# Kernel tuning notes

Measured on AMD Instinct MI355X. Metric: run time of the kernel, lower is better.

The kernel has to match this reference:

```python
import jax, jax.numpy as jnp
import numpy as np

CONF_THRESH = 0.01
TOP_K = 200
NMS_THRESH = 0.45


def setup_inputs() -> dict:
    key = jax.random.key(0)
    k1, k2, k3, k4, k5 = jax.random.split(key, 5)
    B, N, C = 32, 8732, 21
    return {
        "loc_data": jax.random.normal(k1, (B, N, 4), jnp.float32),
        "conf_data": jax.random.normal(k2, (B, N, C), jnp.float32),
        "loc_data2": jax.random.normal(k3, (B, N, 4), jnp.float32),
        "conf_data2": jax.random.normal(k4, (B, N, C), jnp.float32),
        "dbox_list": jax.random.uniform(k5, (N, 4), jnp.float32),
    }


def decode(loc, dbox):
    # SSD decode with variances (0.1, 0.2); loc,dbox: [N,4]; returns xyxy
    cxcy = dbox[:, :2] + loc[:, :2] * 0.1 * dbox[:, 2:]
    wh = dbox[:, 2:] * jnp.exp(loc[:, 2:] * 0.2)
    return jnp.concatenate([cxcy - wh * 0.5, cxcy + wh * 0.5], axis=-1)


def iou_matrix(b):
    # b: [K,4] xyxy -> [K,K] IoU
    x1 = jnp.maximum(b[:, None, 0], b[None, :, 0])
    y1 = jnp.maximum(b[:, None, 1], b[None, :, 1])
    x2 = jnp.minimum(b[:, None, 2], b[None, :, 2])
    y2 = jnp.minimum(b[:, None, 3], b[None, :, 3])
    inter = jnp.clip(x2 - x1, 0.0) * jnp.clip(y2 - y1, 0.0)
    area = (b[:, 2] - b[:, 0]) * (b[:, 3] - b[:, 1])
    union = area[:, None] + area[None, :] - inter
    return inter / union


def nms_class(scores, boxes):
    # scores: [M], boxes: [M,4] for one (image, class)
    masked = jnp.where(scores > CONF_THRESH, scores, -1.0)  # drop sub-threshold
    cand_s, idx = jax.lax.top_k(masked, TOP_K)              # top_k candidate pool
    cand_b = boxes[idx]
    valid = cand_s > CONF_THRESH
    iou = iou_matrix(cand_b)

    def step(suppressed, j):
        keep_j = valid[j] & (~suppressed[j])
        suppressed = suppressed | (keep_j & (iou[j] > NMS_THRESH))
        return suppressed, keep_j

    _, keep = jax.lax.scan(step, jnp.zeros((TOP_K,), bool), jnp.arange(TOP_K))
    entries = jnp.concatenate([cand_s[:, None], cand_b], axis=1)  # [K,5] = (score, box)
    pos = jnp.cumsum(keep) - 1
    pos = jnp.where(keep, pos, TOP_K)  # out-of-bounds -> dropped
    return jnp.zeros((TOP_K, 5), entries.dtype).at[pos].set(entries, mode="drop")


def reference(loc_data, conf_data, loc_data2, conf_data2, dbox_list):
    B, N, _ = loc_data.shape
    C = conf_data.shape[2]
    conf = jax.nn.softmax(conf_data, axis=-1)    # [B,N,C]
    conf2 = jax.nn.softmax(conf_data2, axis=-1)
    boxes1 = jax.vmap(decode, in_axes=(0, None))(loc_data, dbox_list)   # [B,N,4]
    boxes2 = jax.vmap(decode, in_axes=(0, None))(loc_data2, dbox_list)
    # horizontal flip of second (TTA) view: x1' = 1 - x2, x2' = 1 - x1
    boxes2 = jnp.stack(
        [1.0 - boxes2[..., 2], boxes2[..., 1], 1.0 - boxes2[..., 0], boxes2[..., 3]],
        axis=-1,
    )
    boxes = jnp.concatenate([boxes1, boxes2], axis=1)   # [B,2N,4]
    scores = jnp.concatenate([conf, conf2], axis=1)     # [B,2N,C]
    scores = jnp.moveaxis(scores, -1, 1)                # [B,C,2N]
    # vmap over batch and (non-background) classes
    per_class = jax.vmap(jax.vmap(nms_class, in_axes=(0, None)), in_axes=(0, 0))(
        scores[:, 1:], boxes
    )  # [B,C-1,TOP_K,5]
    out = jnp.zeros((B, C, TOP_K, 5), loc_data.dtype)
    return out.at[:, 1:].set(per_class)
```

## Files before the change

### kernel.cpp

```cpp
#include <hip/hip_runtime.h>

#define B_ 32
#define N_ 8732
#define N2_ 17464
#define N4_ 4366
#define C_ 21
#define NCLS 20
#define K_ 200
#define CONF_T 0.01f
#define NMS_T 0.45f
#define TPB_S 256
#define TPB_N 512
#define POOL 1024
#define RANKCAP 512
#define HB0 2048
#define HB 1024
#define BIN0 30791u

typedef unsigned long long u64;
typedef unsigned int u32;

__global__ __launch_bounds__(TPB_S) void softmax_kernel(
    const float* __restrict__ conf1, const float* __restrict__ conf2,
    float* __restrict__ scores)
{
  __shared__ float lds[TPB_S * C_];
  const int t = threadIdx.x;
  const int tile = blockIdx.x * TPB_S;
  const int b = blockIdx.y;
  const int view = blockIdx.z;
  int cnt = N_ - tile; if (cnt > TPB_S) cnt = TPB_S;
  const float* conf = view ? conf2 : conf1;
  const float4* src = (const float4*)(conf + ((size_t)b * N_ + tile) * C_);
  float4* l4 = (float4*)lds;
  const int n4 = (cnt * C_) >> 2;
  for (int i = t; i < n4; i += TPB_S) l4[i] = src[i];
  __syncthreads();
  if (t < cnt) {
    float x[C_];
#pragma unroll
    for (int i = 0; i < C_; ++i) x[i] = lds[t * C_ + i];
    float m = x[0];
#pragma unroll
    for (int i = 1; i < C_; ++i) m = fmaxf(m, x[i]);
    float e[C_];
    float sum = 0.0f;
#pragma unroll
    for (int i = 0; i < C_; ++i) { e[i] = __expf(x[i] - m); sum += e[i]; }
    float inv = 1.0f / sum;
    float* o = scores + ((size_t)b * NCLS) * N2_ + (size_t)view * N_ + (tile + t);
#pragma unroll
    for (int c = 1; c < C_; ++c) { *o = e[c] * inv; o += N2_; }
  }
}

__global__ __launch_bounds__(TPB_N, 2) void nms_kernel(
    const float* __restrict__ scores,
    const float4* __restrict__ loc1,
    const float4* __restrict__ loc2,
    const float4* __restrict__ dbox,
    float* __restrict__ out)
{
  const int t = threadIdx.x;
  const int lane = t & 63;
  const int wv = t >> 6;
  const int bimg = blockIdx.x / NCLS;
  const int cls = 1 + (blockIdx.x % NCLS);
  const float4* sc4 = (const float4*)(scores + ((size_t)bimg * NCLS + (cls - 1)) * N2_);
  float* ob = out + ((size_t)bimg * C_ + cls) * K_ * 5;

  __shared__ u32 hist[HB0];
  __shared__ u64 pool[POOL] __attribute__((aligned(16)));
  __shared__ u64 spool[256];
  __shared__ float4 bb[K_];
  __shared__ float bar[K_];
  __shared__ u64 rowmask[K_][4];
  __shared__ u64 validmask[4];
  __shared__ u32 wtot[8];
  __shared__ u32 sh_sel, sh_Sb, sh_Sn, sh_nc;

  {
    const float4 z4 = make_float4(0.f, 0.f, 0.f, 0.f);
    if (t < 250) ((float4*)ob)[t] = z4;
    if (cls == 1 && t >= 256 && t < 506)
      ((float4*)(out + (size_t)bimg * C_ * K_ * 5))[t - 256] = z4;
  }

  float4 v[9];
#pragma unroll
  for (int k = 0; k < 9; ++k) {
    int i = t + k * TPB_N;
    v[k] = (i < N4_) ? sc4[i] : make_float4(0.f, 0.f, 0.f, 0.f);
  }

  hist[t] = 0u; hist[t + 512] = 0u; hist[t + 1024] = 0u; hist[t + 1536] = 0u;
  pool[t] = 0ULL; pool[t + TPB_N] = 0ULL;
  if (t == 0) sh_nc = 0u;
  __syncthreads();

#pragma unroll
  for (int k = 0; k < 9; ++k) {
    float ss[4] = {v[k].x, v[k].y, v[k].z, v[k].w};
#pragma unroll
    for (int c2 = 0; c2 < 4; ++c2) {
      float s = ss[c2];
      if (s > CONF_T)
        atomicAdd(&hist[(__float_as_uint(s) >> 15) - BIN0], 1u);
    }
  }
  __syncthreads();

  {
    u32 c0 = hist[4 * t + 0], c1 = hist[4 * t + 1];
    u32 c2b = hist[4 * t + 2], c3 = hist[4 * t + 3];
    u32 T = c0 + c1 + c2b + c3;
    u32 x = T;
#pragma unroll
    for (int off = 1; off < 64; off <<= 1) {
      u32 y = __shfl_down(x, off);
      if (lane + off < 64) x += y;
    }
    if (lane == 0) wtot[wv] = x;
    __syncthreads();
    u32 wafter = 0;
    for (int w = wv + 1; w < 8; ++w) wafter += wtot[w];
    u32 after_me = (x - T) + wafter;
    u32 S3 = c3 + after_me, S2 = c2b + S3, S1 = c1 + S2, S0 = c0 + S1;
    hist[4 * t + 0] = S0; hist[4 * t + 1] = S1;
    hist[4 * t + 2] = S2; hist[4 * t + 3] = S3;
  }
  __syncthreads();

  u32 loKey, prefix = 0, Gacc = 0;
  bool needMore = false;
  {
    u32 total = hist[0];
    if (total < (u32)K_) {
      loKey = 1u;
    } else {
      for (int h = t; h < HB0; h += TPB_N) {
        u32 Sb = hist[h];
        u32 Sn = (h + 1 < HB0) ? hist[h + 1] : 0u;
        if (Sb >= (u32)K_ && Sn < (u32)K_) { sh_sel = (u32)h; sh_Sb = Sb; sh_Sn = Sn; }
      }
      __syncthreads();
      prefix = sh_sel + BIN0;
      loKey = prefix << 15;
      Gacc = sh_Sn;
      needMore = sh_Sb > (u32)RANKCAP;
    }
  }

  for (int lvl = 1; lvl <= 2 && needMore; ++lvl) {
    const int shift = (lvl == 1) ? 5 : 0;
    const int mshift = (lvl == 1) ? 15 : 5;
    const u32 bmask = (lvl == 1) ? 1023u : 31u;
    for (int h = t; h < HB; h += TPB_N) hist[h] = 0u;
    __syncthreads();
#pragma unroll
    for (int k = 0; k < 9; ++k) {
      float ss[4] = {v[k].x, v[k].y, v[k].z, v[k].w};
#pragma unroll
      for (int c2 = 0; c2 < 4; ++c2) {
        float s = ss[c2];
        if (s > CONF_T) {
          u32 key = __float_as_uint(s);
          if ((key >> mshift) == prefix)
            atomicAdd(&hist[(key >> shift) & bmask], 1u);
        }
      }
    }
    __syncthreads();
    u32 c0 = hist[2 * t], c1 = hist[2 * t + 1];
    u32 T = c0 + c1;
    u32 x = T;
#pragma unroll
    for (int off = 1; off < 64; off <<= 1) {
      u32 y = __shfl_down(x, off);
      if (lane + off < 64) x += y;
    }
    if (lane == 0) wtot[wv] = x;
    __syncthreads();
    u32 wafter = 0;
    for (int w = wv + 1; w < 8; ++w) wafter += wtot[w];
    u32 after_me = (x - T) + wafter;
    u32 S1 = c1 + after_me, S0 = c0 + S1;
    hist[2 * t] = S0; hist[2 * t + 1] = S1;
    __syncthreads();
    u32 need = (u32)K_ - Gacc;
    for (int h = t; h < HB; h += TPB_N) {
      u32 Sb = hist[h];
      u32 Sn2 = (h + 1 < HB) ? hist[h + 1] : 0u;
      if (Sb >= need && Sn2 < need) { sh_sel = (u32)h; sh_Sb = Sb; sh_Sn = Sn2; }
    }
    __syncthreads();
    prefix = (prefix << ((lvl == 1) ? 10 : 5)) | sh_sel;
    u32 candTotal = Gacc + sh_Sb;
    Gacc += sh_Sn;
    loKey = prefix << shift;
    needMore = (candTotal > (u32)RANKCAP) && (lvl < 2);
  }

#pragma unroll
  for (int k = 0; k < 9; ++k) {
    int i = t + k * TPB_N;
    float ss[4] = {v[k].x, v[k].y, v[k].z, v[k].w};
#pragma unroll
    for (int c2 = 0; c2 < 4; ++c2) {
      float s = ss[c2];
      u32 key = __float_as_uint(s);
      bool pred = (s > CONF_T) && (key >= loKey);
      u64 bal = __ballot(pred);
      if (bal) {
        u32 wb = 0;
        if (lane == 0) wb = atomicAdd(&sh_nc, (u32)__popcll(bal));
        wb = __shfl(wb, 0);
        if (pred) {
          u32 pos = wb + (u32)__popcll(bal & ((1ULL << lane) - 1ULL));
          if (pos < (u32)POOL)
            pool[pos] = ((u64)key << 32) | (u64)(0xFFFFFFFFu - (u32)(i * 4 + c2));
        }
      }
    }
  }
  __syncthreads();

  u32 nc = sh_nc < (u32)POOL ? sh_nc : (u32)POOL;
  if (t < 256) spool[t] = 0ULL;
  const bool dual = nc > (u32)TPB_N;
  u64 my0 = (t < (int)nc) ? pool[t] : 0ULL;
  u64 my1 = (dual && t + TPB_N < (int)nc) ? pool[t + TPB_N] : 0ULL;
  __syncthreads();
  u32 r0 = 0, r1 = 0;
  if ((u32)(t & ~63) < nc) {
    if (!dual) {
#pragma unroll 4
      for (u32 k = 0; k < nc; k += 2) {
        ulonglong2 pk = *(const ulonglong2*)&pool[k];
        r0 += (pk.x > my0) ? 1u : 0u;
        r0 += (pk.y > my0) ? 1u : 0u;
      }
    } else {
#pragma unroll 4
      for (u32 k = 0; k < nc; k += 2) {
        ulonglong2 pk = *(const ulonglong2*)&pool[k];
        r0 += (pk.x > my0) ? 1u : 0u;
        r0 += (pk.y > my0) ? 1u : 0u;
        r1 += (pk.x > my1) ? 1u : 0u;
        r1 += (pk.y > my1) ? 1u : 0u;
      }
    }
  }
  if (my0 != 0ULL && r0 < (u32)K_) spool[r0] = my0;
  if (dual && my1 != 0ULL && r1 < (u32)K_) spool[r1] = my1;
  __syncthreads();

  float scv = 0.f;
  if (t < K_) {
    float x1 = 0.f, y1 = 0.f, x2 = 0.f, y2 = 0.f, area = 0.f;
    u64 e = spool[t];
    u32 kb = (u32)(e >> 32);
    if (kb != 0u) {
      scv = __uint_as_float(kb);
      u32 idx = 0xFFFFFFFFu - (u32)(e & 0xFFFFFFFFu);
      int nn = (idx < (u32)N_) ? (int)idx : (int)(idx - N_);
      float4 l = (idx < (u32)N_) ? loc1[(size_t)bimg * N_ + nn]
                                 : loc2[(size_t)bimg * N_ + nn];
      float4 d = dbox[nn];
      float cx = d.x + l.x * 0.1f * d.z;
      float cy = d.y + l.y * 0.1f * d.w;
      float w = d.z * __expf(l.z * 0.2f);
      float h = d.w * __expf(l.w * 0.2f);
      x1 = cx - w * 0.5f; y1 = cy - h * 0.5f;
      x2 = cx + w * 0.5f; y2 = cy + h * 0.5f;
      if (idx >= (u32)N_) {
        float tmp = 1.0f - x2; x2 = 1.0f - x1; x1 = tmp;
      }
      area = (x2 - x1) * (y2 - y1);
    }
    bb[t] = make_float4(x1, y1, x2, y2);
    bar[t] = area;
  } else if (t >= 256) {
    for (int i = t - 256; i < 4 * K_; i += 256) ((u64*)rowmask)[i] = 0ULL;
  }
  {
    bool myvalid = (t < K_) && (scv > CONF_T);
    u64 bal = __ballot(myvalid);
    if (lane == 0 && wv < 4) validmask[wv] = bal;
  }
  __syncthreads();

  if (t < 2 * K_) {
    const int j = (t < K_) ? t : (t - K_);
    const int h = (t < K_) ? 0 : 1;
    const int L = K_ - 1 - j;
    const int half = (L + 1) >> 1;
    const int s0c = j + 1 + (h ? half : 0);
    const int e0c = h ? K_ : (j + 1 + half);
    if (s0c < e0c) {
      float4 mb = bb[j];
      float ma = bar[j];
      for (int w = (s0c >> 6); w <= ((e0c - 1) >> 6); ++w) {
        int ka = (w << 6) > s0c ? (w << 6) : s0c;
        int kb2 = ((w + 1) << 6) < e0c ? ((w + 1) << 6) : e0c;
        u64 m = 0ULL;
        for (int k2 = ka; k2 < kb2; ++k2) {
          float4 obx = bb[k2];
          float ox1 = fmaxf(mb.x, obx.x);
          float oy1 = fmaxf(mb.y, obx.y);
          float ox2 = fminf(mb.z, obx.z);
          float oy2 = fminf(mb.w, obx.w);
          float inter = fmaxf(ox2 - ox1, 0.f) * fmaxf(oy2 - oy1, 0.f);
          float uni = ma + bar[k2] - inter;
          m |= (inter > NMS_T * uni) ? (1ULL << (k2 & 63)) : 0ULL;
        }
        if (m) atomicOr(&rowmask[j][w], m);
      }
    }
  }
  __syncthreads();

  if (t < 64) {
    const u64 vv0 = validmask[0], vv1 = validmask[1];
    const u64 vv2 = validmask[2], vv3 = validmask[3];
    u64 s0 = 0, s1 = 0, s2 = 0, s3 = 0;
    u64 k0 = 0, k1 = 0, k2m = 0, k3 = 0;
#pragma unroll 8
    for (int j = 0; j < 64; ++j) {
      u64 q0 = rowmask[j][0], q1 = rowmask[j][1], q2 = rowmask[j][2], q3 = rowmask[j][3];
      u64 bit = 1ULL << j;
      if ((vv0 & bit) && !(s0 & bit)) { s0 |= q0; s1 |= q1; s2 |= q2; s3 |= q3; k0 |= bit; }
    }
#pragma unroll 8
    for (int j = 64; j < 128; ++j) {
      u64 q1 = rowmask[j][1], q2 = rowmask[j][2], q3 = rowmask[j][3];
      u64 bit = 1ULL << (j & 63);
      if ((vv1 & bit) && !(s1 & bit)) { s1 |= q1; s2 |= q2; s3 |= q3; k1 |= bit; }
    }
#pragma unroll 8
    for (int j = 128; j < 192; ++j) {
      u64 q2 = rowmask[j][2], q3 = rowmask[j][3];
      u64 bit = 1ULL << (j & 63);
      if ((vv2 & bit) && !(s2 & bit)) { s2 |= q2; s3 |= q3; k2m |= bit; }
    }
#pragma unroll
    for (int j = 192; j < K_; ++j) {
      u64 q3 = rowmask[j][3];
      u64 bit = 1ULL << (j & 63);
      if ((vv3 & bit) && !(s3 & bit)) { s3 |= q3; k3 |= bit; }
    }
    const u32 n0 = (u32)__popcll(k0);
    const u32 n01 = n0 + (u32)__popcll(k1);
    const u32 n012 = n01 + (u32)__popcll(k2m);
    const u64 below = (1ULL << lane) - 1ULL;
#pragma unroll
    for (int w = 0; w < 4; ++w) {
      int j = (w << 6) + lane;
      if (j < K_) {
        u64 kw = (w == 0) ? k0 : (w == 1) ? k1 : (w == 2) ? k2m : k3;
        if ((kw >> lane) & 1ULL) {
          int pos2 = (int)__popcll(kw & below)
                  + (int)((w == 0) ? 0u : (w == 1) ? n0 : (w == 2) ? n01 : n012);
          u64 e = spool[j];
          float sc = __uint_as_float((u32)(e >> 32));
          float4 bx = bb[j];
          float* o = ob + (size_t)pos2 * 5;
          o[0] = sc; o[1] = bx.x; o[2] = bx.y; o[3] = bx.z; o[4] = bx.w;
        }
      }
    }
  }
}

extern "C" void kernel_launch(void* const* d_in, const int* in_sizes, int n_in,
                              void* d_out, int out_size, void* d_ws, size_t ws_size,
                              hipStream_t stream) {
  const float* loc1 = (const float*)d_in[0];
  const float* conf1 = (const float*)d_in[1];
  const float* loc2 = (const float*)d_in[2];
  const float* conf2 = (const float*)d_in[3];
  const float* dbox = (const float*)d_in[4];
  float* out = (float*)d_out;
  float* scores = (float*)d_ws;

  dim3 g1((N_ + TPB_S - 1) / TPB_S, B_, 2);
  softmax_kernel<<<g1, TPB_S, 0, stream>>>(conf1, conf2, scores);

  nms_kernel<<<B_ * NCLS, TPB_N, 0, stream>>>(
      scores, (const float4*)loc1, (const float4*)loc2, (const float4*)dbox, out);
}
```

Measured before the change: 151.6 us.

## Replace radix refinement with histogram-bucketed scatter and per-bucket ranking

```diff
diff --git a/kernel.cpp b/kernel.cpp
--- a/kernel.cpp
+++ b/kernel.cpp
@@ -131,12 +131,13 @@
   }
   __syncthreads();
 
-  u32 loKey, prefix = 0, Gacc = 0;
-  bool needMore = false;
+  u32 loKey, selBin = 0, ncand, prefix = 0, Gacc = 0;
+  bool fallback = false;
   {
     u32 total = hist[0];
     if (total < (u32)K_) {
       loKey = 1u;
+      ncand = total;
     } else {
       for (int h = t; h < HB0; h += TPB_N) {
         u32 Sb = hist[h];
@@ -144,115 +145,144 @@
         if (Sb >= (u32)K_ && Sn < (u32)K_) { sh_sel = (u32)h; sh_Sb = Sb; sh_Sn = Sn; }
       }
       __syncthreads();
+      selBin = sh_sel;
       prefix = sh_sel + BIN0;
       loKey = prefix << 15;
+      ncand = sh_Sb;
       Gacc = sh_Sn;
-      needMore = sh_Sb > (u32)RANKCAP;
-    }
-  }
-
-  for (int lvl = 1; lvl <= 2 && needMore; ++lvl) {
-    const int shift = (lvl == 1) ? 5 : 0;
-    const int mshift = (lvl == 1) ? 15 : 5;
-    const u32 bmask = (lvl == 1) ? 1023u : 31u;
-    for (int h = t; h < HB; h += TPB_N) hist[h] = 0u;
-    __syncthreads();
+      fallback = sh_Sb > (u32)POOL;
+    }
+  }
+
+  if (t < 256) spool[t] = 0ULL;
+
+  if (!fallback) {
 #pragma unroll
     for (int k = 0; k < 9; ++k) {
+      int i = t + k * TPB_N;
       float ss[4] = {v[k].x, v[k].y, v[k].z, v[k].w};
 #pragma unroll
       for (int c2 = 0; c2 < 4; ++c2) {
         float s = ss[c2];
-        if (s > CONF_T) {
-          u32 key = __float_as_uint(s);
-          if ((key >> mshift) == prefix)
-            atomicAdd(&hist[(key >> shift) & bmask], 1u);
+        u32 key = __float_as_uint(s);
+        if (s > CONF_T && key >= loKey) {
+          u32 h = (key >> 15) - BIN0;
+          u32 pos = atomicSub(&hist[h], 1u) - 1u;
+          pool[pos] = ((u64)key << 32) | (u64)(0xFFFFFFFFu - (u32)(i * 4 + c2));
         }
       }
     }
     __syncthreads();
-    u32 c0 = hist[2 * t], c1 = hist[2 * t + 1];
-    u32 T = c0 + c1;
-    u32 x = T;
-#pragma unroll
-    for (int off = 1; off < 64; off <<= 1) {
-      u32 y = __shfl_down(x, off);
-      if (lane + off < 64) x += y;
-    }
-    if (lane == 0) wtot[wv] = x;
+    for (int slot = t; slot < (int)ncand; slot += TPB_N) {
+      u64 e = pool[slot];
+      u32 h = ((u32)(e >> 32) >> 15) - BIN0;
+      u32 base = hist[h];
+      u32 up = (h == selBin) ? ncand : hist[h - 1];
+      u32 r = base;
+      for (u32 q = base; q < up; ++q) r += (pool[q] > e) ? 1u : 0u;
+      if (r < (u32)K_) spool[r] = e;
+    }
+  } else {
+    bool needMore = true;
+    for (int lvl = 1; lvl <= 2 && needMore; ++lvl) {
+      const int shift = (lvl == 1) ? 5 : 0;
+      const int mshift = (lvl == 1) ? 15 : 5;
+      const u32 bmask = (lvl == 1) ? 1023u : 31u;
+      for (int h = t; h < HB; h += TPB_N) hist[h] = 0u;
+      __syncthreads();
+#pragma unroll
+      for (int k = 0; k < 9; ++k) {
+        float ss[4] = {v[k].x, v[k].y, v[k].z, v[k].w};
+#pragma unroll
+        for (int c2 = 0; c2 < 4; ++c2) {
+          float s = ss[c2];
+          if (s > CONF_T) {
+            u32 key = __float_as_uint(s);
+            if ((key >> mshift) == prefix)
+              atomicAdd(&hist[(key >> shift) & bmask], 1u);
+          }
+        }
+      }
+      __syncthreads();
+      u32 c0 = hist[2 * t], c1 = hist[2 * t + 1];
+      u32 T = c0 + c1;
+      u32 x = T;
+#pragma unroll
+      for (int off = 1; off < 64; off <<= 1) {
+        u32 y = __shfl_down(x, off);
+        if (lane + off < 64) x += y;
+      }
+      if (lane == 0) wtot[wv] = x;
+      __syncthreads();
+      u32 wafter = 0;
+      for (int w = wv + 1; w < 8; ++w) wafter += wtot[w];
+      u32 after_me = (x - T) + wafter;
+      u32 S1 = c1 + after_me, S0 = c0 + S1;
+      hist[2 * t] = S0; hist[2 * t + 1] = S1;
+      __syncthreads();
+      u32 need = (u32)K_ - Gacc;
+      for (int h = t; h < HB; h += TPB_N) {
+        u32 Sb = hist[h];
+        u32 Sn2 = (h + 1 < HB) ? hist[h + 1] : 0u;
+        if (Sb >= need && Sn2 < need) { sh_sel = (u32)h; sh_Sb = Sb; sh_Sn = Sn2; }
+      }
+      __syncthreads();
+      prefix = (prefix << ((lvl == 1) ? 10 : 5)) | sh_sel;
+      u32 candTotal = Gacc + sh_Sb;
+      Gacc += sh_Sn;
+      loKey = prefix << shift;
+      needMore = (candTotal > (u32)RANKCAP) && (lvl < 2);
+    }
+#pragma unroll
+    for (int k = 0; k < 9; ++k) {
+      int i = t + k * TPB_N;
+      float ss[4] = {v[k].x, v[k].y, v[k].z, v[k].w};
+#pragma unroll
+      for (int c2 = 0; c2 < 4; ++c2) {
+        float s = ss[c2];
+        u32 key = __float_as_uint(s);
+        bool pred = (s > CONF_T) && (key >= loKey);
+        u64 bal = __ballot(pred);
+        if (bal) {
+          u32 wb = 0;
+          if (lane == 0) wb = atomicAdd(&sh_nc, (u32)__popcll(bal));
+          wb = __shfl(wb, 0);
+          if (pred) {
+            u32 pos = wb + (u32)__popcll(bal & ((1ULL << lane) - 1ULL));
+            if (pos < (u32)POOL)
+              pool[pos] = ((u64)key << 32) | (u64)(0xFFFFFFFFu - (u32)(i * 4 + c2));
+          }
+        }
+      }
+    }
     __syncthreads();
-    u32 wafter = 0;
-    for (int w = wv + 1; w < 8; ++w) wafter += wtot[w];
-    u32 after_me = (x - T) + wafter;
-    u32 S1 = c1 + after_me, S0 = c0 + S1;
-    hist[2 * t] = S0; hist[2 * t + 1] = S1;
-    __syncthreads();
-    u32 need = (u32)K_ - Gacc;
-    for (int h = t; h < HB; h += TPB_N) {
-      u32 Sb = hist[h];
-      u32 Sn2 = (h + 1 < HB) ? hist[h + 1] : 0u;
-      if (Sb >= need && Sn2 < need) { sh_sel = (u32)h; sh_Sb = Sb; sh_Sn = Sn2; }
-    }
-    __syncthreads();
-    prefix = (prefix << ((lvl == 1) ? 10 : 5)) | sh_sel;
-    u32 candTotal = Gacc + sh_Sb;
-    Gacc += sh_Sn;
-    loKey = prefix << shift;
-    needMore = (candTotal > (u32)RANKCAP) && (lvl < 2);
-  }
-
-#pragma unroll
-  for (int k = 0; k < 9; ++k) {
-    int i = t + k * TPB_N;
-    float ss[4] = {v[k].x, v[k].y, v[k].z, v[k].w};
-#pragma unroll
-    for (int c2 = 0; c2 < 4; ++c2) {
-      float s = ss[c2];
-      u32 key = __float_as_uint(s);
-      bool pred = (s > CONF_T) && (key >= loKey);
-      u64 bal = __ballot(pred);
-      if (bal) {
-        u32 wb = 0;
-        if (lane == 0) wb = atomicAdd(&sh_nc, (u32)__popcll(bal));
-        wb = __shfl(wb, 0);
-        if (pred) {
-          u32 pos = wb + (u32)__popcll(bal & ((1ULL << lane) - 1ULL));
-          if (pos < (u32)POOL)
-            pool[pos] = ((u64)key << 32) | (u64)(0xFFFFFFFFu - (u32)(i * 4 + c2));
-        }
-      }
-    }
-  }
-  __syncthreads();
-
-  u32 nc = sh_nc < (u32)POOL ? sh_nc : (u32)POOL;
-  if (t < 256) spool[t] = 0ULL;
-  const bool dual = nc > (u32)TPB_N;
-  u64 my0 = (t < (int)nc) ? pool[t] : 0ULL;
-  u64 my1 = (dual && t + TPB_N < (int)nc) ? pool[t + TPB_N] : 0ULL;
-  __syncthreads();
-  u32 r0 = 0, r1 = 0;
-  if ((u32)(t & ~63) < nc) {
-    if (!dual) {
+    u32 nc = sh_nc < (u32)POOL ? sh_nc : (u32)POOL;
+    const bool dual = nc > (u32)TPB_N;
+    u64 my0 = (t < (int)nc) ? pool[t] : 0ULL;
+    u64 my1 = (dual && t + TPB_N < (int)nc) ? pool[t + TPB_N] : 0ULL;
+    u32 r0 = 0, r1 = 0;
+    if ((u32)(t & ~63) < nc) {
+      if (!dual) {
 #pragma unroll 4
-      for (u32 k = 0; k < nc; k += 2) {
-        ulonglong2 pk = *(const ulonglong2*)&pool[k];
-        r0 += (pk.x > my0) ? 1u : 0u;
-        r0 += (pk.y > my0) ? 1u : 0u;
-      }
-    } else {
+        for (u32 k = 0; k < nc; k += 2) {
+          ulonglong2 pk = *(const ulonglong2*)&pool[k];
+          r0 += (pk.x > my0) ? 1u : 0u;
+          r0 += (pk.y > my0) ? 1u : 0u;
+        }
+      } else {
 #pragma unroll 4
-      for (u32 k = 0; k < nc; k += 2) {
-        ulonglong2 pk = *(const ulonglong2*)&pool[k];
-        r0 += (pk.x > my0) ? 1u : 0u;
-        r0 += (pk.y > my0) ? 1u : 0u;
-        r1 += (pk.x > my1) ? 1u : 0u;
-        r1 += (pk.y > my1) ? 1u : 0u;
-      }
-    }
-  }
-  if (my0 != 0ULL && r0 < (u32)K_) spool[r0] = my0;
-  if (dual && my1 != 0ULL && r1 < (u32)K_) spool[r1] = my1;
+        for (u32 k = 0; k < nc; k += 2) {
+          ulonglong2 pk = *(const ulonglong2*)&pool[k];
+          r0 += (pk.x > my0) ? 1u : 0u;
+          r0 += (pk.y > my0) ? 1u : 0u;
+          r1 += (pk.x > my1) ? 1u : 0u;
+          r1 += (pk.y > my1) ? 1u : 0u;
+        }
+      }
+    }
+    if (my0 != 0ULL && r0 < (u32)K_) spool[r0] = my0;
+    if (dual && my1 != 0ULL && r1 < (u32)K_) spool[r1] = my1;
+  }
   __syncthreads();
 
   float scv = 0.f;
```

After: 145.3 us. -4.1%, faster.

## Make NMS kernel persistent with atomic work-stealing over image-class items

Applied to the files above, without the earlier changes.

```diff
diff --git a/kernel.cpp b/kernel.cpp
--- a/kernel.cpp
+++ b/kernel.cpp
@@ -7,6 +7,8 @@
 #define C_ 21
 #define NCLS 20
 #define K_ 200
+#define NITEMS 640
+#define PGRID 512
 #define CONF_T 0.01f
 #define NMS_T 0.45f
 #define TPB_S 256
@@ -22,13 +24,14 @@
 
 __global__ __launch_bounds__(TPB_S) void softmax_kernel(
     const float* __restrict__ conf1, const float* __restrict__ conf2,
-    float* __restrict__ scores)
+    float* __restrict__ scores, u32* gcnt)
 {
   __shared__ float lds[TPB_S * C_];
   const int t = threadIdx.x;
   const int tile = blockIdx.x * TPB_S;
   const int b = blockIdx.y;
   const int view = blockIdx.z;
+  if (gcnt && t == 0 && tile == 0 && b == 0 && view == 0) *gcnt = 0u;
   int cnt = N_ - tile; if (cnt > TPB_S) cnt = TPB_S;
   const float* conf = view ? conf2 : conf1;
   const float4* src = (const float4*)(conf + ((size_t)b * N_ + tile) * C_);
@@ -59,15 +62,11 @@
     const float4* __restrict__ loc1,
     const float4* __restrict__ loc2,
     const float4* __restrict__ dbox,
-    float* __restrict__ out)
+    float* __restrict__ out, u32* gcnt)
 {
   const int t = threadIdx.x;
   const int lane = t & 63;
   const int wv = t >> 6;
-  const int bimg = blockIdx.x / NCLS;
-  const int cls = 1 + (blockIdx.x % NCLS);
-  const float4* sc4 = (const float4*)(scores + ((size_t)bimg * NCLS + (cls - 1)) * N2_);
-  float* ob = out + ((size_t)bimg * C_ + cls) * K_ * 5;
 
   __shared__ u32 hist[HB0];
   __shared__ u64 pool[POOL] __attribute__((aligned(16)));
@@ -77,298 +76,313 @@
   __shared__ u64 rowmask[K_][4];
   __shared__ u64 validmask[4];
   __shared__ u32 wtot[8];
-  __shared__ u32 sh_sel, sh_Sb, sh_Sn, sh_nc;
-
-  {
-    const float4 z4 = make_float4(0.f, 0.f, 0.f, 0.f);
-    if (t < 250) ((float4*)ob)[t] = z4;
-    if (cls == 1 && t >= 256 && t < 506)
-      ((float4*)(out + (size_t)bimg * C_ * K_ * 5))[t - 256] = z4;
-  }
-
-  float4 v[9];
-#pragma unroll
-  for (int k = 0; k < 9; ++k) {
-    int i = t + k * TPB_N;
-    v[k] = (i < N4_) ? sc4[i] : make_float4(0.f, 0.f, 0.f, 0.f);
-  }
-
-  hist[t] = 0u; hist[t + 512] = 0u; hist[t + 1024] = 0u; hist[t + 1536] = 0u;
-  pool[t] = 0ULL; pool[t + TPB_N] = 0ULL;
-  if (t == 0) sh_nc = 0u;
-  __syncthreads();
-
-#pragma unroll
-  for (int k = 0; k < 9; ++k) {
-    float ss[4] = {v[k].x, v[k].y, v[k].z, v[k].w};
-#pragma unroll
-    for (int c2 = 0; c2 < 4; ++c2) {
-      float s = ss[c2];
-      if (s > CONF_T)
-        atomicAdd(&hist[(__float_as_uint(s) >> 15) - BIN0], 1u);
-    }
-  }
-  __syncthreads();
-
-  {
-    u32 c0 = hist[4 * t + 0], c1 = hist[4 * t + 1];
-    u32 c2b = hist[4 * t + 2], c3 = hist[4 * t + 3];
-    u32 T = c0 + c1 + c2b + c3;
-    u32 x = T;
-#pragma unroll
-    for (int off = 1; off < 64; off <<= 1) {
-      u32 y = __shfl_down(x, off);
-      if (lane + off < 64) x += y;
-    }
-    if (lane == 0) wtot[wv] = x;
-    __syncthreads();
-    u32 wafter = 0;
-    for (int w = wv + 1; w < 8; ++w) wafter += wtot[w];
-    u32 after_me = (x - T) + wafter;
-    u32 S3 = c3 + after_me, S2 = c2b + S3, S1 = c1 + S2, S0 = c0 + S1;
-    hist[4 * t + 0] = S0; hist[4 * t + 1] = S1;
-    hist[4 * t + 2] = S2; hist[4 * t + 3] = S3;
-  }
-  __syncthreads();
-
-  u32 loKey, prefix = 0, Gacc = 0;
-  bool needMore = false;
-  {
-    u32 total = hist[0];
-    if (total < (u32)K_) {
-      loKey = 1u;
-    } else {
-      for (int h = t; h < HB0; h += TPB_N) {
-        u32 Sb = hist[h];
-        u32 Sn = (h + 1 < HB0) ? hist[h + 1] : 0u;
-        if (Sb >= (u32)K_ && Sn < (u32)K_) { sh_sel = (u32)h; sh_Sb = Sb; sh_Sn = Sn; }
-      }
-      __syncthreads();
-      prefix = sh_sel + BIN0;
-      loKey = prefix << 15;
-      Gacc = sh_Sn;
-      needMore = sh_Sb > (u32)RANKCAP;
-    }
-  }
-
-  for (int lvl = 1; lvl <= 2 && needMore; ++lvl) {
-    const int shift = (lvl == 1) ? 5 : 0;
-    const int mshift = (lvl == 1) ? 15 : 5;
-    const u32 bmask = (lvl == 1) ? 1023u : 31u;
-    for (int h = t; h < HB; h += TPB_N) hist[h] = 0u;
-    __syncthreads();
+  __shared__ u32 sh_sel, sh_Sb, sh_Sn, sh_nc, sh_item;
+
+  u32 item = blockIdx.x;
+
+  while (true) {
+    const int bimg = (int)(item / NCLS);
+    const int cls = 1 + (int)(item % NCLS);
+    const float4* sc4 = (const float4*)(scores + ((size_t)bimg * NCLS + (cls - 1)) * N2_);
+    float* ob = out + ((size_t)bimg * C_ + cls) * K_ * 5;
+
+    {
+      const float4 z4 = make_float4(0.f, 0.f, 0.f, 0.f);
+      if (t < 250) ((float4*)ob)[t] = z4;
+      if (cls == 1 && t >= 256 && t < 506)
+        ((float4*)(out + (size_t)bimg * C_ * K_ * 5))[t - 256] = z4;
+    }
+
+    float4 v[9];
+#pragma unroll
+    for (int k = 0; k < 9; ++k) {
+      int i = t + k * TPB_N;
+      v[k] = (i < N4_) ? sc4[i] : make_float4(0.f, 0.f, 0.f, 0.f);
+    }
+
+    hist[t] = 0u; hist[t + 512] = 0u; hist[t + 1024] = 0u; hist[t + 1536] = 0u;
+    pool[t] = 0ULL; pool[t + TPB_N] = 0ULL;
+    if (t == 0) sh_nc = 0u;
+    __syncthreads();
+
 #pragma unroll
     for (int k = 0; k < 9; ++k) {
       float ss[4] = {v[k].x, v[k].y, v[k].z, v[k].w};
 #pragma unroll
       for (int c2 = 0; c2 < 4; ++c2) {
         float s = ss[c2];
-        if (s > CONF_T) {
-          u32 key = __float_as_uint(s);
-          if ((key >> mshift) == prefix)
-            atomicAdd(&hist[(key >> shift) & bmask], 1u);
-        }
-      }
-    }
-    __syncthreads();
-    u32 c0 = hist[2 * t], c1 = hist[2 * t + 1];
-    u32 T = c0 + c1;
-    u32 x = T;
-#pragma unroll
-    for (int off = 1; off < 64; off <<= 1) {
-      u32 y = __shfl_down(x, off);
-      if (lane + off < 64) x += y;
-    }
-    if (lane == 0) wtot[wv] = x;
-    __syncthreads();
-    u32 wafter = 0;
-    for (int w = wv + 1; w < 8; ++w) wafter += wtot[w];
-    u32 after_me = (x - T) + wafter;
-    u32 S1 = c1 + after_me, S0 = c0 + S1;
-    hist[2 * t] = S0; hist[2 * t + 1] = S1;
-    __syncthreads();
-    u32 need = (u32)K_ - Gacc;
-    for (int h = t; h < HB; h += TPB_N) {
-      u32 Sb = hist[h];
-      u32 Sn2 = (h + 1 < HB) ? hist[h + 1] : 0u;
-      if (Sb >= need && Sn2 < need) { sh_sel = (u32)h; sh_Sb = Sb; sh_Sn = Sn2; }
-    }
-    __syncthreads();
-    prefix = (prefix << ((lvl == 1) ? 10 : 5)) | sh_sel;
-    u32 candTotal = Gacc + sh_Sb;
-    Gacc += sh_Sn;
-    loKey = prefix << shift;
-    needMore = (candTotal > (u32)RANKCAP) && (lvl < 2);
-  }
-
-#pragma unroll
-  for (int k = 0; k < 9; ++k) {
-    int i = t + k * TPB_N;
-    float ss[4] = {v[k].x, v[k].y, v[k].z, v[k].w};
-#pragma unroll
-    for (int c2 = 0; c2 < 4; ++c2) {
-      float s = ss[c2];
-      u32 key = __float_as_uint(s);
-      bool pred = (s > CONF_T) && (key >= loKey);
-      u64 bal = __ballot(pred);
-      if (bal) {
-        u32 wb = 0;
-        if (lane == 0) wb = atomicAdd(&sh_nc, (u32)__popcll(bal));
-        wb = __shfl(wb, 0);
-        if (pred) {
-          u32 pos = wb + (u32)__popcll(bal & ((1ULL << lane) - 1ULL));
-          if (pos < (u32)POOL)
-            pool[pos] = ((u64)key << 32) | (u64)(0xFFFFFFFFu - (u32)(i * 4 + c2));
-        }
-      }
-    }
-  }
-  __syncthreads();
-
-  u32 nc = sh_nc < (u32)POOL ? sh_nc : (u32)POOL;
-  if (t < 256) spool[t] = 0ULL;
-  const bool dual = nc > (u32)TPB_N;
-  u64 my0 = (t < (int)nc) ? pool[t] : 0ULL;
-  u64 my1 = (dual && t + TPB_N < (int)nc) ? pool[t + TPB_N] : 0ULL;
-  __syncthreads();
-  u32 r0 = 0, r1 = 0;
-  if ((u32)(t & ~63) < nc) {
-    if (!dual) {
+        if (s > CONF_T)
+          atomicAdd(&hist[(__float_as_uint(s) >> 15) - BIN0], 1u);
+      }
+    }
+    __syncthreads();
+
+    {
+      u32 c0 = hist[4 * t + 0], c1 = hist[4 * t + 1];
+      u32 c2b = hist[4 * t + 2], c3 = hist[4 * t + 3];
+      u32 T = c0 + c1 + c2b + c3;
+      u32 x = T;
+#pragma unroll
+      for (int off = 1; off < 64; off <<= 1) {
+        u32 y = __shfl_down(x, off);
+        if (lane + off < 64) x += y;
+      }
+      if (lane == 0) wtot[wv] = x;
+      __syncthreads();
+      u32 wafter = 0;
+      for (int w = wv + 1; w < 8; ++w) wafter += wtot[w];
+      u32 after_me = (x - T) + wafter;
+      u32 S3 = c3 + after_me, S2 = c2b + S3, S1 = c1 + S2, S0 = c0 + S1;
+      hist[4 * t + 0] = S0; hist[4 * t + 1] = S1;
+      hist[4 * t + 2] = S2; hist[4 * t + 3] = S3;
+    }
+    __syncthreads();
+
+    u32 loKey, prefix = 0, Gacc = 0;
+    bool needMore = false;
+    {
+      u32 total = hist[0];
+      if (total < (u32)K_) {
+        loKey = 1u;
+      } else {
+        for (int h = t; h < HB0; h += TPB_N) {
+          u32 Sb = hist[h];
+          u32 Sn = (h + 1 < HB0) ? hist[h + 1] : 0u;
+          if (Sb >= (u32)K_ && Sn < (u32)K_) { sh_sel = (u32)h; sh_Sb = Sb; sh_Sn = Sn; }
+        }
+        __syncthreads();
+        prefix = sh_sel + BIN0;
+        loKey = prefix << 15;
+        Gacc = sh_Sn;
+        needMore = sh_Sb > (u32)RANKCAP;
+      }
+    }
+
+    for (int lvl = 1; lvl <= 2 && needMore; ++lvl) {
+      const int shift = (lvl == 1) ? 5 : 0;
+      const int mshift = (lvl == 1) ? 15 : 5;
+      const u32 bmask = (lvl == 1) ? 1023u : 31u;
+      for (int h = t; h < HB; h += TPB_N) hist[h] = 0u;
+      __syncthreads();
+#pragma unroll
+      for (int k = 0; k < 9; ++k) {
+        float ss[4] = {v[k].x, v[k].y, v[k].z, v[k].w};
+#pragma unroll
+        for (int c2 = 0; c2 < 4; ++c2) {
+          float s = ss[c2];
+          if (s > CONF_T) {
+            u32 key = __float_as_uint(s);
+            if ((key >> mshift) == prefix)
+              atomicAdd(&hist[(key >> shift) & bmask], 1u);
+          }
+        }
+      }
+      __syncthreads();
+      u32 c0 = hist[2 * t], c1 = hist[2 * t + 1];
+      u32 T = c0 + c1;
+      u32 x = T;
+#pragma unroll
+      for (int off = 1; off < 64; off <<= 1) {
+        u32 y = __shfl_down(x, off);
+        if (lane + off < 64) x += y;
+      }
+      if (lane == 0) wtot[wv] = x;
+      __syncthreads();
+      u32 wafter = 0;
+      for (int w = wv + 1; w < 8; ++w) wafter += wtot[w];
+      u32 after_me = (x - T) + wafter;
+      u32 S1 = c1 + after_me, S0 = c0 + S1;
+      hist[2 * t] = S0; hist[2 * t + 1] = S1;
+      __syncthreads();
+      u32 need = (u32)K_ - Gacc;
+      for (int h = t; h < HB; h += TPB_N) {
+        u32 Sb = hist[h];
+        u32 Sn2 = (h + 1 < HB) ? hist[h + 1] : 0u;
+        if (Sb >= need && Sn2 < need) { sh_sel = (u32)h; sh_Sb = Sb; sh_Sn = Sn2; }
+      }
+      __syncthreads();
+      prefix = (prefix << ((lvl == 1) ? 10 : 5)) | sh_sel;
+      u32 candTotal = Gacc + sh_Sb;
+      Gacc += sh_Sn;
+      loKey = prefix << shift;
+      needMore = (candTotal > (u32)RANKCAP) && (lvl < 2);
+    }
+
+#pragma unroll
+    for (int k = 0; k < 9; ++k) {
+      int i = t + k * TPB_N;
+      float ss[4] = {v[k].x, v[k].y, v[k].z, v[k].w};
+#pragma unroll
+      for (int c2 = 0; c2 < 4; ++c2) {
+        float s = ss[c2];
+        u32 key = __float_as_uint(s);
+        bool pred = (s > CONF_T) && (key >= loKey);
+        u64 bal = __ballot(pred);
+        if (bal) {
+          u32 wb = 0;
+          if (lane == 0) wb = atomicAdd(&sh_nc, (u32)__popcll(bal));
+          wb = __shfl(wb, 0);
+          if (pred) {
+            u32 pos = wb + (u32)__popcll(bal & ((1ULL << lane) - 1ULL));
+            if (pos < (u32)POOL)
+              pool[pos] = ((u64)key << 32) | (u64)(0xFFFFFFFFu - (u32)(i * 4 + c2));
+          }
+        }
+      }
+    }
+    __syncthreads();
+
+    u32 nc = sh_nc < (u32)POOL ? sh_nc : (u32)POOL;
+    if (t < 256) spool[t] = 0ULL;
+    const bool dual = nc > (u32)TPB_N;
+    u64 my0 = (t < (int)nc) ? pool[t] : 0ULL;
+    u64 my1 = (dual && t + TPB_N < (int)nc) ? pool[t + TPB_N] : 0ULL;
+    __syncthreads();
+    u32 r0 = 0, r1 = 0;
+    if ((u32)(t & ~63) < nc) {
+      if (!dual) {
 #pragma unroll 4
-      for (u32 k = 0; k < nc; k += 2) {
-        ulonglong2 pk = *(const ulonglong2*)&pool[k];
-        r0 += (pk.x > my0) ? 1u : 0u;
-        r0 += (pk.y > my0) ? 1u : 0u;
-      }
-    } else {
+        for (u32 k = 0; k < nc; k += 2) {
+          ulonglong2 pk = *(const ulonglong2*)&pool[k];
+          r0 += (pk.x > my0) ? 1u : 0u;
+          r0 += (pk.y > my0) ? 1u : 0u;
+        }
+      } else {
 #pragma unroll 4
-      for (u32 k = 0; k < nc; k += 2) {
-        ulonglong2 pk = *(const ulonglong2*)&pool[k];
-        r0 += (pk.x > my0) ? 1u : 0u;
-        r0 += (pk.y > my0) ? 1u : 0u;
-        r1 += (pk.x > my1) ? 1u : 0u;
-        r1 += (pk.y > my1) ? 1u : 0u;
-      }
-    }
-  }
-  if (my0 != 0ULL && r0 < (u32)K_) spool[r0] = my0;
-  if (dual && my1 != 0ULL && r1 < (u32)K_) spool[r1] = my1;
-  __syncthreads();
-
-  float scv = 0.f;
-  if (t < K_) {
-    float x1 = 0.f, y1 = 0.f, x2 = 0.f, y2 = 0.f, area = 0.f;
-    u64 e = spool[t];
-    u32 kb = (u32)(e >> 32);
-    if (kb != 0u) {
-      scv = __uint_as_float(kb);
-      u32 idx = 0xFFFFFFFFu - (u32)(e & 0xFFFFFFFFu);
-      int nn = (idx < (u32)N_) ? (int)idx : (int)(idx - N_);
-      float4 l = (idx < (u32)N_) ? loc1[(size_t)bimg * N_ + nn]
-                                 : loc2[(size_t)bimg * N_ + nn];
-      float4 d = dbox[nn];
-      float cx = d.x + l.x * 0.1f * d.z;
-      float cy = d.y + l.y * 0.1f * d.w;
-      float w = d.z * __expf(l.z * 0.2f);
-      float h = d.w * __expf(l.w * 0.2f);
-      x1 = cx - w * 0.5f; y1 = cy - h * 0.5f;
-      x2 = cx + w * 0.5f; y2 = cy + h * 0.5f;
-      if (idx >= (u32)N_) {
-        float tmp = 1.0f - x2; x2 = 1.0f - x1; x1 = tmp;
-      }
-      area = (x2 - x1) * (y2 - y1);
-    }
-    bb[t] = make_float4(x1, y1, x2, y2);
-    bar[t] = area;
-  } else if (t >= 256) {
-    for (int i = t - 256; i < 4 * K_; i += 256) ((u64*)rowmask)[i] = 0ULL;
-  }
-  {
-    bool myvalid = (t < K_) && (scv > CONF_T);
-    u64 bal = __ballot(myvalid);
-    if (lane == 0 && wv < 4) validmask[wv] = bal;
-  }
-  __syncthreads();
-
-  if (t < 2 * K_) {
-    const int j = (t < K_) ? t : (t - K_);
-    const int h = (t < K_) ? 0 : 1;
-    const int L = K_ - 1 - j;
-    const int half = (L + 1) >> 1;
-    const int s0c = j + 1 + (h ? half : 0);
-    const int e0c = h ? K_ : (j + 1 + half);
-    if (s0c < e0c) {
-      float4 mb = bb[j];
-      float ma = bar[j];
-      for (int w = (s0c >> 6); w <= ((e0c - 1) >> 6); ++w) {
-        int ka = (w << 6) > s0c ? (w << 6) : s0c;
-        int kb2 = ((w + 1) << 6) < e0c ? ((w + 1) << 6) : e0c;
-        u64 m = 0ULL;
-        for (int k2 = ka; k2 < kb2; ++k2) {
-          float4 obx = bb[k2];
-          float ox1 = fmaxf(mb.x, obx.x);
-          float oy1 = fmaxf(mb.y, obx.y);
-          float ox2 = fminf(mb.z, obx.z);
-          float oy2 = fminf(mb.w, obx.w);
-          float inter = fmaxf(ox2 - ox1, 0.f) * fmaxf(oy2 - oy1, 0.f);
-          float uni = ma + bar[k2] - inter;
-          m |= (inter > NMS_T * uni) ? (1ULL << (k2 & 63)) : 0ULL;
-        }
-        if (m) atomicOr(&rowmask[j][w], m);
-      }
-    }
-  }
-  __syncthreads();
-
-  if (t < 64) {
-    const u64 vv0 = validmask[0], vv1 = validmask[1];
-    const u64 vv2 = validmask[2], vv3 = validmask[3];
-    u64 s0 = 0, s1 = 0, s2 = 0, s3 = 0;
-    u64 k0 = 0, k1 = 0, k2m = 0, k3 = 0;
+        for (u32 k = 0; k < nc; k += 2) {
+          ulonglong2 pk = *(const ulonglong2*)&pool[k];
+          r0 += (pk.x > my0) ? 1u : 0u;
+          r0 += (pk.y > my0) ? 1u : 0u;
+          r1 += (pk.x > my1) ? 1u : 0u;
+          r1 += (pk.y > my1) ? 1u : 0u;
+        }
+      }
+    }
+    if (my0 != 0ULL && r0 < (u32)K_) spool[r0] = my0;
+    if (dual && my1 != 0ULL && r1 < (u32)K_) spool[r1] = my1;
+    __syncthreads();
+
+    float scv = 0.f;
+    if (t < K_) {
+      float x1 = 0.f, y1 = 0.f, x2 = 0.f, y2 = 0.f, area = 0.f;
+      u64 e = spool[t];
+      u32 kb = (u32)(e >> 32);
+      if (kb != 0u) {
+        scv = __uint_as_float(kb);
+        u32 idx = 0xFFFFFFFFu - (u32)(e & 0xFFFFFFFFu);
+        int nn = (idx < (u32)N_) ? (int)idx : (int)(idx - N_);
+        float4 l = (idx < (u32)N_) ? loc1[(size_t)bimg * N_ + nn]
+                                   : loc2[(size_t)bimg * N_ + nn];
+        float4 d = dbox[nn];
+        float cx = d.x + l.x * 0.1f * d.z;
+        float cy = d.y + l.y * 0.1f * d.w;
+        float w = d.z * __expf(l.z * 0.2f);
+        float h = d.w * __expf(l.w * 0.2f);
+        x1 = cx - w * 0.5f; y1 = cy - h * 0.5f;
+        x2 = cx + w * 0.5f; y2 = cy + h * 0.5f;
+        if (idx >= (u32)N_) {
+          float tmp = 1.0f - x2; x2 = 1.0f - x1; x1 = tmp;
+        }
+        area = (x2 - x1) * (y2 - y1);
+      }
+      bb[t] = make_float4(x1, y1, x2, y2);
+      bar[t] = area;
+    } else if (t >= 256) {
+      for (int i = t - 256; i < 4 * K_; i += 256) ((u64*)rowmask)[i] = 0ULL;
+    }
+    {
+      bool myvalid = (t < K_) && (scv > CONF_T);
+      u64 bal = __ballot(myvalid);
+      if (lane == 0 && wv < 4) validmask[wv] = bal;
+    }
+    __syncthreads();
+
+    if (t < 2 * K_) {
+      const int j = (t < K_) ? t : (t - K_);
+      const int h = (t < K_) ? 0 : 1;
+      const int L = K_ - 1 - j;
+      const int half = (L + 1) >> 1;
+      const int s0c = j + 1 + (h ? half : 0);
+      const int e0c = h ? K_ : (j + 1 + half);
+      if (s0c < e0c) {
+        float4 mb = bb[j];
+        float ma = bar[j];
+        for (int w = (s0c >> 6); w <= ((e0c - 1) >> 6); ++w) {
+          int ka = (w << 6) > s0c ? (w << 6) : s0c;
+          int kb2 = ((w + 1) << 6) < e0c ? ((w + 1) << 6) : e0c;
+          u64 m = 0ULL;
+          for (int k2 = ka; k2 < kb2; ++k2) {
+            float4 obx = bb[k2];
+            float ox1 = fmaxf(mb.x, obx.x);
+            float oy1 = fmaxf(mb.y, obx.y);
+            float ox2 = fminf(mb.z, obx.z);
+            float oy2 = fminf(mb.w, obx.w);
+            float inter = fmaxf(ox2 - ox1, 0.f) * fmaxf(oy2 - oy1, 0.f);
+            float uni = ma + bar[k2] - inter;
+            m |= (inter > NMS_T * uni) ? (1ULL << (k2 & 63)) : 0ULL;
+          }
+          if (m) atomicOr(&rowmask[j][w], m);
+        }
+      }
+    }
+    __syncthreads();
+
+    if (t < 64) {
+      const u64 vv0 = validmask[0], vv1 = validmask[1];
+      const u64 vv2 = validmask[2], vv3 = validmask[3];
+      u64 s0 = 0, s1 = 0, s2 = 0, s3 = 0;
+      u64 k0 = 0, k1 = 0, k2m = 0, k3 = 0;
 #pragma unroll 8
-    for (int j = 0; j < 64; ++j) {
-      u64 q0 = rowmask[j][0], q1 = rowmask[j][1], q2 = rowmask[j][2], q3 = rowmask[j][3];
-      u64 bit = 1ULL << j;
-      if ((vv0 & bit) && !(s0 & bit)) { s0 |= q0; s1 |= q1; s2 |= q2; s3 |= q3; k0 |= bit; }
-    }
+      for (int j = 0; j < 64; ++j) {
+        u64 q0 = rowmask[j][0], q1 = rowmask[j][1], q2 = rowmask[j][2], q3 = rowmask[j][3];
+        u64 bit = 1ULL << j;
+        if ((vv0 & bit) && !(s0 & bit)) { s0 |= q0; s1 |= q1; s2 |= q2; s3 |= q3; k0 |= bit; }
+      }
 #pragma unroll 8
-    for (int j = 64; j < 128; ++j) {
-      u64 q1 = rowmask[j][1], q2 = rowmask[j][2], q3 = rowmask[j][3];
-      u64 bit = 1ULL << (j & 63);
-      if ((vv1 & bit) && !(s1 & bit)) { s1 |= q1; s2 |= q2; s3 |= q3; k1 |= bit; }
-    }
+      for (int j = 64; j < 128; ++j) {
+        u64 q1 = rowmask[j][1], q2 = rowmask[j][2], q3 = rowmask[j][3];
+        u64 bit = 1ULL << (j & 63);
+        if ((vv1 & bit) && !(s1 & bit)) { s1 |= q1; s2 |= q2; s3 |= q3; k1 |= bit; }
+      }
 #pragma unroll 8
-    for (int j = 128; j < 192; ++j) {
-      u64 q2 = rowmask[j][2], q3 = rowmask[j][3];
-      u64 bit = 1ULL << (j & 63);
-      if ((vv2 & bit) && !(s2 & bit)) { s2 |= q2; s3 |= q3; k2m |= bit; }
-    }
-#pragma unroll
-    for (int j = 192; j < K_; ++j) {
-      u64 q3 = rowmask[j][3];
-      u64 bit = 1ULL << (j & 63);
-      if ((vv3 & bit) && !(s3 & bit)) { s3 |= q3; k3 |= bit; }
-    }
-    const u32 n0 = (u32)__popcll(k0);
-    const u32 n01 = n0 + (u32)__popcll(k1);
-    const u32 n012 = n01 + (u32)__popcll(k2m);
-    const u64 below = (1ULL << lane) - 1ULL;
-#pragma unroll
-    for (int w = 0; w < 4; ++w) {
-      int j = (w << 6) + lane;
-      if (j < K_) {
-        u64 kw = (w == 0) ? k0 : (w == 1) ? k1 : (w == 2) ? k2m : k3;
-        if ((kw >> lane) & 1ULL) {
-          int pos2 = (int)__popcll(kw & below)
-                  + (int)((w == 0) ? 0u : (w == 1) ? n0 : (w == 2) ? n01 : n012);
-          u64 e = spool[j];
-          float sc = __uint_as_float((u32)(e >> 32));
-          float4 bx = bb[j];
-          float* o = ob + (size_t)pos2 * 5;
-          o[0] = sc; o[1] = bx.x; o[2] = bx.y; o[3] = bx.z; o[4] = bx.w;
-        }
-      }
-    }
+      for (int j = 128; j < 192; ++j) {
+        u64 q2 = rowmask[j][2], q3 = rowmask[j][3];
+        u64 bit = 1ULL << (j & 63);
+        if ((vv2 & bit) && !(s2 & bit)) { s2 |= q2; s3 |= q3; k2m |= bit; }
+      }
+#pragma unroll
+      for (int j = 192; j < K_; ++j) {
+        u64 q3 = rowmask[j][3];
+        u64 bit = 1ULL << (j & 63);
+        if ((vv3 & bit) && !(s3 & bit)) { s3 |= q3; k3 |= bit; }
+      }
+      const u32 n0 = (u32)__popcll(k0);
+      const u32 n01 = n0 + (u32)__popcll(k1);
+      const u32 n012 = n01 + (u32)__popcll(k2m);
+      const u64 below = (1ULL << lane) - 1ULL;
+#pragma unroll
+      for (int w = 0; w < 4; ++w) {
+        int j = (w << 6) + lane;
+        if (j < K_) {
+          u64 kw = (w == 0) ? k0 : (w == 1) ? k1 : (w == 2) ? k2m : k3;
+          if ((kw >> lane) & 1ULL) {
+            int pos2 = (int)__popcll(kw & below)
+                    + (int)((w == 0) ? 0u : (w == 1) ? n0 : (w == 2) ? n01 : n012);
+            u64 e = spool[j];
+            float sc = __uint_as_float((u32)(e >> 32));
+            float4 bx = bb[j];
+            float* o = ob + (size_t)pos2 * 5;
+            o[0] = sc; o[1] = bx.x; o[2] = bx.y; o[3] = bx.z; o[4] = bx.w;
+          }
+        }
+      }
+    }
+
+    if (t == 0)
+      sh_item = gcnt ? ((u32)PGRID + atomicAdd(gcnt, 1u)) : 0xFFFFFFFFu;
+    __syncthreads();
+    item = sh_item;
+    if (item >= (u32)NITEMS) break;
   }
 }
 
@@ -383,9 +397,18 @@
   float* out = (float*)d_out;
   float* scores = (float*)d_ws;
 
+  const size_t SCORES_BYTES = (size_t)B_ * NCLS * N2_ * sizeof(float);
+  u32* gcnt = nullptr;
+  int grid = NITEMS;
+  if (ws_size >= SCORES_BYTES + sizeof(u32)) {
+    gcnt = (u32*)((char*)d_ws + SCORES_BYTES);
+    grid = PGRID;
+  }
+
   dim3 g1((N_ + TPB_S - 1) / TPB_S, B_, 2);
-  softmax_kernel<<<g1, TPB_S, 0, stream>>>(conf1, conf2, scores);
-
-  nms_kernel<<<B_ * NCLS, TPB_N, 0, stream>>>(
-      scores, (const float4*)loc1, (const float4*)loc2, (const float4*)dbox, out);
+  softmax_kernel<<<g1, TPB_S, 0, stream>>>(conf1, conf2, scores, gcnt);
+
+  nms_kernel<<<grid, TPB_N, 0, stream>>>(
+      scores, (const float4*)loc1, (const float4*)loc2, (const float4*)dbox,
+      out, gcnt);
 }
```

Measured after the change: 217.9 us. 43.7% more time.

## Fuse threshold-bin search into prefix scans and compact pool via block scan

Applied to the files above, without the earlier changes.

```diff
diff --git a/kernel.cpp b/kernel.cpp
--- a/kernel.cpp
+++ b/kernel.cpp
@@ -77,7 +77,7 @@
   __shared__ u64 rowmask[K_][4];
   __shared__ u64 validmask[4];
   __shared__ u32 wtot[8];
-  __shared__ u32 sh_sel, sh_Sb, sh_Sn, sh_nc;
+  __shared__ u32 sh_sel, sh_Sb, sh_Sn, sh_nc, sh_total;
 
   {
     const float4 z4 = make_float4(0.f, 0.f, 0.f, 0.f);
@@ -95,7 +95,7 @@
 
   hist[t] = 0u; hist[t + 512] = 0u; hist[t + 1024] = 0u; hist[t + 1536] = 0u;
   pool[t] = 0ULL; pool[t + TPB_N] = 0ULL;
-  if (t == 0) sh_nc = 0u;
+  if (t < 256) spool[t] = 0ULL;
   __syncthreads();
 
 #pragma unroll
@@ -125,25 +125,23 @@
     u32 wafter = 0;
     for (int w = wv + 1; w < 8; ++w) wafter += wtot[w];
     u32 after_me = (x - T) + wafter;
-    u32 S3 = c3 + after_me, S2 = c2b + S3, S1 = c1 + S2, S0 = c0 + S1;
-    hist[4 * t + 0] = S0; hist[4 * t + 1] = S1;
-    hist[4 * t + 2] = S2; hist[4 * t + 3] = S3;
+    u32 S4 = after_me;
+    u32 S3 = c3 + S4, S2 = c2b + S3, S1 = c1 + S2, S0 = c0 + S1;
+    if (t == 0) sh_total = S0;
+    if (S0 >= (u32)K_ && S1 < (u32)K_) { sh_sel = 4u * t + 0u; sh_Sb = S0; sh_Sn = S1; }
+    if (S1 >= (u32)K_ && S2 < (u32)K_) { sh_sel = 4u * t + 1u; sh_Sb = S1; sh_Sn = S2; }
+    if (S2 >= (u32)K_ && S3 < (u32)K_) { sh_sel = 4u * t + 2u; sh_Sb = S2; sh_Sn = S3; }
+    if (S3 >= (u32)K_ && S4 < (u32)K_) { sh_sel = 4u * t + 3u; sh_Sb = S3; sh_Sn = S4; }
   }
   __syncthreads();
 
   u32 loKey, prefix = 0, Gacc = 0;
   bool needMore = false;
   {
-    u32 total = hist[0];
+    u32 total = sh_total;
     if (total < (u32)K_) {
       loKey = 1u;
     } else {
-      for (int h = t; h < HB0; h += TPB_N) {
-        u32 Sb = hist[h];
-        u32 Sn = (h + 1 < HB0) ? hist[h + 1] : 0u;
-        if (Sb >= (u32)K_ && Sn < (u32)K_) { sh_sel = (u32)h; sh_Sb = Sb; sh_Sn = Sn; }
-      }
-      __syncthreads();
       prefix = sh_sel + BIN0;
       loKey = prefix << 15;
       Gacc = sh_Sn;
@@ -184,15 +182,11 @@
     u32 wafter = 0;
     for (int w = wv + 1; w < 8; ++w) wafter += wtot[w];
     u32 after_me = (x - T) + wafter;
-    u32 S1 = c1 + after_me, S0 = c0 + S1;
-    hist[2 * t] = S0; hist[2 * t + 1] = S1;
-    __syncthreads();
+    u32 S2 = after_me;
+    u32 S1 = c1 + S2, S0 = c0 + S1;
     u32 need = (u32)K_ - Gacc;
-    for (int h = t; h < HB; h += TPB_N) {
-      u32 Sb = hist[h];
-      u32 Sn2 = (h + 1 < HB) ? hist[h + 1] : 0u;
-      if (Sb >= need && Sn2 < need) { sh_sel = (u32)h; sh_Sb = Sb; sh_Sn = Sn2; }
-    }
+    if (S0 >= need && S1 < need) { sh_sel = 2u * t + 0u; sh_Sb = S0; sh_Sn = S1; }
+    if (S1 >= need && S2 < need) { sh_sel = 2u * t + 1u; sh_Sb = S1; sh_Sn = S2; }
     __syncthreads();
     prefix = (prefix << ((lvl == 1) ? 10 : 5)) | sh_sel;
     u32 candTotal = Gacc + sh_Sb;
@@ -201,24 +195,39 @@
     needMore = (candTotal > (u32)RANKCAP) && (lvl < 2);
   }
 
-#pragma unroll
-  for (int k = 0; k < 9; ++k) {
-    int i = t + k * TPB_N;
-    float ss[4] = {v[k].x, v[k].y, v[k].z, v[k].w};
-#pragma unroll
-    for (int c2 = 0; c2 < 4; ++c2) {
-      float s = ss[c2];
-      u32 key = __float_as_uint(s);
-      bool pred = (s > CONF_T) && (key >= loKey);
-      u64 bal = __ballot(pred);
-      if (bal) {
-        u32 wb = 0;
-        if (lane == 0) wb = atomicAdd(&sh_nc, (u32)__popcll(bal));
-        wb = __shfl(wb, 0);
-        if (pred) {
-          u32 pos = wb + (u32)__popcll(bal & ((1ULL << lane) - 1ULL));
+  {
+    u32 mycnt = 0;
+#pragma unroll
+    for (int k = 0; k < 9; ++k) {
+      float ss[4] = {v[k].x, v[k].y, v[k].z, v[k].w};
+#pragma unroll
+      for (int c2 = 0; c2 < 4; ++c2)
+        mycnt += (ss[c2] > CONF_T && __float_as_uint(ss[c2]) >= loKey) ? 1u : 0u;
+    }
+    u32 inc = mycnt;
+#pragma unroll
+    for (int off = 1; off < 64; off <<= 1) {
+      u32 y = __shfl_up(inc, off);
+      if (lane >= off) inc += y;
+    }
+    if (lane == 63) wtot[wv] = inc;
+    __syncthreads();
+    u32 wbase = 0;
+    for (int w = 0; w < wv; ++w) wbase += wtot[w];
+    u32 pos = wbase + (inc - mycnt);
+    if (t == TPB_N - 1) sh_nc = wbase + inc;
+#pragma unroll
+    for (int k = 0; k < 9; ++k) {
+      int i = t + k * TPB_N;
+      float ss[4] = {v[k].x, v[k].y, v[k].z, v[k].w};
+#pragma unroll
+      for (int c2 = 0; c2 < 4; ++c2) {
+        float s = ss[c2];
+        u32 key = __float_as_uint(s);
+        if (s > CONF_T && key >= loKey) {
           if (pos < (u32)POOL)
             pool[pos] = ((u64)key << 32) | (u64)(0xFFFFFFFFu - (u32)(i * 4 + c2));
+          ++pos;
         }
       }
     }
@@ -226,11 +235,9 @@
   __syncthreads();
 
   u32 nc = sh_nc < (u32)POOL ? sh_nc : (u32)POOL;
-  if (t < 256) spool[t] = 0ULL;
   const bool dual = nc > (u32)TPB_N;
   u64 my0 = (t < (int)nc) ? pool[t] : 0ULL;
   u64 my1 = (dual && t + TPB_N < (int)nc) ? pool[t + TPB_N] : 0ULL;
-  __syncthreads();
   u32 r0 = 0, r1 = 0;
   if ((u32)(t & ~63) < nc) {
     if (!dual) {
```

Measured after the change: 151.0 us (median of 2 runs). No clear change (-0.4%).
